# Kernel optimization log

Hardware: AMD Instinct MI355X
Metric: run time of the kernel (lower is better)

The kernel has to match this reference:

```python
import jax, jax.numpy as jnp
import numpy as np


def setup_inputs() -> dict:
    key = jax.random.key(0)
    k1, k2, k3, k4 = jax.random.split(key, 4)
    B, N, dim, heads, dim_head = 4, 1025, 768, 12, 64
    inner = heads * dim_head
    x = jax.random.normal(k1, (B, N, dim), dtype=jnp.float32)
    # binary occlusion mask over the N-1 patch tokens (CLS handled inside forward)
    mask = (jax.random.uniform(k2, (B, N - 1, dim)) > 0.5).astype(jnp.float32)
    w_qkv = jax.random.normal(k3, (inner * 3, dim), dtype=jnp.float32) * 0.02
    w_out = jax.random.normal(k4, (dim, inner), dtype=jnp.float32) * 0.02
    b_out = jnp.zeros((dim,), dtype=jnp.float32)
    return {"x": x, "mask": mask, "w_qkv": w_qkv, "w_out": w_out, "b_out": b_out, "heads": heads}


def reference(x, mask, w_qkv, w_out, b_out, heads):
    B, N, dim = x.shape
    inner = w_qkv.shape[0] // 3
    d = inner // heads
    scale = d ** -0.5

    def split_heads(t):  # [B, n, h*d] -> [B, h, n, d]
        return t.reshape(B, t.shape[1], heads, d).transpose(0, 2, 1, 3)

    qkv = x @ w_qkv.T  # [B, N, 3*inner]
    q, k, v = map(split_heads, jnp.split(qkv, 3, axis=-1))

    # --- mask propagation (torch.no_grad block) ---
    mask_sg = jax.lax.stop_gradient(mask)
    qkv_m = mask_sg @ jax.lax.stop_gradient(jnp.abs(w_qkv)).T  # [B, N-1, 3*inner]

    def norm_mask(t):
        t = split_heads(t)  # [B, h, N-1, d]
        t = t / (1e-6 + jnp.max(t, axis=2, keepdims=True))
        return jnp.concatenate([jnp.ones_like(t[:, :, :1]), t], axis=2)  # [B, h, N, d]

    q_m, k_m, v_m = map(norm_mask, jnp.split(qkv_m, 3, axis=-1))
    updated = (jnp.mean(mask_sg, axis=-1, keepdims=True) > 0.0).astype(x.dtype)  # [B, N-1, 1]
    updated = jnp.concatenate([jnp.ones_like(updated[:, :1]), updated], axis=1)  # [B, N, 1]

    # --- masked attention ---
    dots = jnp.einsum('bhnd,bhmd->bhnm', q * q_m, k * k_m) * scale
    attn = jax.nn.softmax(dots, axis=-1)
    out = jnp.einsum('bhnm,bhmd->bhnd', attn, v_m * v)
    out = out.transpose(0, 2, 1, 3).reshape(B, N, inner) * updated
    out = out @ w_out.T + b_out

    # --- mask output propagation (no grad) ---
    m = jax.lax.stop_gradient(jnp.einsum('bhnm,bhmd->bhnd', attn, v_m))
    m = m.transpose(0, 2, 1, 3).reshape(B, N, inner) * updated
    m = m @ jax.lax.stop_gradient(jnp.abs(w_out)).T
    return (out, m[:, 1:])
```

## Files before the change

### kernel.cpp

```cpp
#include <hip/hip_runtime.h>
#include <cmath>

#define TPB 256

static const int NTOK  = 1025;
static const int DIM   = 768;
static const int HEADS = 12;
static const int QK3   = 2304;
static const int ROWS  = 4 * NTOK;
static const int MROWS = 4 * (NTOK - 1);
static const int MPAD  = 4224;
static const int NPAD  = 1088;
static const size_t OUT0 = (size_t)ROWS * DIM;
static const size_t APLANE = (size_t)MPAD * DIM;

static const size_t OFF_QKV16  = 0;
static const size_t OFF_QKVM16 = 4800000;
static const size_t OFF_QE     = 9600000;
static const size_t OFF_KF     = 11300000;
static const size_t OFF_VF     = 13000000;
static const size_t OFF_ABF    = 16400000;
static const size_t OFF_WQ     = 19700000;
static const size_t OFF_WO     = 21500000;
static const size_t OFF_CMAX   = 22100000;
static const size_t OFF_UPD    = 22110000;

typedef __attribute__((ext_vector_type(8))) short short8;
typedef __attribute__((ext_vector_type(4))) float f32x4;

__device__ __forceinline__ unsigned short f2bf(float f) {
    union { float f; unsigned int u; } c; c.f = f;
    unsigned int u = c.u + 0x7fffu + ((c.u >> 16) & 1u);
    return (unsigned short)(u >> 16);
}
__device__ __forceinline__ float bf2f(unsigned short u) {
    union { unsigned int u; float f; } c; c.u = (unsigned int)u << 16;
    return c.f;
}
__device__ __forceinline__ unsigned int cvtpk(float a, float b) {
    unsigned int r;
    asm("v_cvt_pk_bf16_f32 %0, %1, %2" : "=v"(r) : "v"(a), "v"(b));
    return r;
}
__device__ __forceinline__ void gl_lds16(const unsigned short* g, unsigned short* l) {
    __builtin_amdgcn_global_load_lds(
        (const __attribute__((address_space(1))) unsigned int*)g,
        (__attribute__((address_space(3))) unsigned int*)l, 16, 0, 0);
}

__global__ __launch_bounds__(TPB)
void k_cvt(const float* __restrict__ x, const float* __restrict__ mask,
           const float* __restrict__ wqkv, const float* __restrict__ wout,
           unsigned short* __restrict__ Abf, unsigned short* __restrict__ Wq,
           unsigned short* __restrict__ Wo)
{
    const int z = blockIdx.z;
    const size_t idx = ((size_t)blockIdx.x * TPB + threadIdx.x) * 8;
    unsigned short o[8] __attribute__((aligned(16)));
    if (z <= 1) {
        if (idx >= APLANE) return;
        const int row = (int)(idx / DIM);
        const int M = z ? MROWS : ROWS;
        const float* src = z ? mask : x;
        if (row < M) {
            float a[8];
            *(float4*)&a[0] = *(const float4*)(src + idx);
            *(float4*)&a[4] = *(const float4*)(src + idx + 4);
#pragma unroll
            for (int i = 0; i < 8; ++i) o[i] = f2bf(a[i]);
        } else {
#pragma unroll
            for (int i = 0; i < 8; ++i) o[i] = 0;
        }
        *(short8*)(Abf + (size_t)z * APLANE + idx) = *(short8*)o;
    } else {
        const size_t tot = (z == 2) ? (size_t)QK3 * DIM : (size_t)DIM * DIM;
        if (idx >= tot) return;
        const float* src = (z == 2) ? wqkv : wout;
        unsigned short* dst = (z == 2) ? Wq : Wo;
        float a[8];
        *(float4*)&a[0] = *(const float4*)(src + idx);
        *(float4*)&a[4] = *(const float4*)(src + idx + 4);
        unsigned short oa[8] __attribute__((aligned(16)));
#pragma unroll
        for (int i = 0; i < 8; ++i) { o[i] = f2bf(a[i]); oa[i] = f2bf(fabsf(a[i])); }
        *(short8*)(dst + idx) = *(short8*)o;
        *(short8*)(dst + tot + idx) = *(short8*)oa;
    }
}

__global__ __launch_bounds__(TPB)
void k_gemm_qkv_mfma(const unsigned short* __restrict__ Abf,
                     const unsigned short* __restrict__ Wq,
                     unsigned short* __restrict__ qkv16,
                     unsigned short* __restrict__ qkvm16,
                     float* __restrict__ cmax)
{
    const int bid = blockIdx.x;
    const int xcd = bid & 7, rr = bid >> 3;
    const int id = (xcd < 4) ? (xcd * 149 + rr) : (596 + (xcd - 4) * 148 + rr);
    const int z = id / 594;
    const int rem = id - z * 594;
    const int by = rem / 18, bx = rem - by * 18;
    const int rowT = by * 128, colT = bx * 128;
    if (z == 1 && rowT >= MROWS) return;
    const unsigned short* A = Abf + (size_t)z * APLANE;
    const unsigned short* B = Wq + (size_t)z * QK3 * DIM;

    __shared__ unsigned short As[2][128 * 64];
    __shared__ unsigned short Bs[2][128 * 64];

    const int t = threadIdx.x;
    const int w = t >> 6, lane = t & 63, l15 = lane & 15, quad = lane >> 4;
    const int wm = (w & 1) * 64, wn = (w >> 1) * 64;
    const int sr = t >> 2, sk = (t & 3) * 8;

    f32x4 acc[4][4];
#pragma unroll
    for (int i = 0; i < 4; ++i)
#pragma unroll
        for (int j = 0; j < 4; ++j) acc[i][j] = (f32x4){0.f, 0.f, 0.f, 0.f};

    auto stage = [&](int buf, int k0) {
#pragma unroll
        for (int c = 0; c < 4; ++c) {
            const int gr = sr + (c & 1) * 64;
            const int gk = k0 + (c >> 1) * 32 + sk;
            gl_lds16(A + (size_t)(rowT + gr) * DIM + gk, As[buf] + c * 2048 + t * 8);
            gl_lds16(B + (size_t)(colT + gr) * DIM + gk, Bs[buf] + c * 2048 + t * 8);
        }
    };

    stage(0, 0);
    for (int kt = 0; kt < 12; ++kt) {
        const int cur = kt & 1;
        if (kt < 11) {
            stage(cur ^ 1, (kt + 1) * 64);
            asm volatile("s_waitcnt vmcnt(8)" ::: "memory");
        } else {
            asm volatile("s_waitcnt vmcnt(0)" ::: "memory");
        }
        __builtin_amdgcn_s_barrier();
        __builtin_amdgcn_sched_barrier(0);
        short8 fa[2][4], fb[2][4];
#pragma unroll
        for (int kk = 0; kk < 2; ++kk) {
#pragma unroll
            for (int mi = 0; mi < 4; ++mi)
                fa[kk][mi] = *(const short8*)(As[cur] + kk * 4096 + (wm + mi * 16 + l15) * 32 + quad * 8);
#pragma unroll
            for (int ni = 0; ni < 4; ++ni)
                fb[kk][ni] = *(const short8*)(Bs[cur] + kk * 4096 + (wn + ni * 16 + l15) * 32 + quad * 8);
        }
        __builtin_amdgcn_s_setprio(1);
#pragma unroll
        for (int kk = 0; kk < 2; ++kk)
#pragma unroll
            for (int mi = 0; mi < 4; ++mi)
#pragma unroll
                for (int ni = 0; ni < 4; ++ni)
                    acc[mi][ni] = __builtin_amdgcn_mfma_f32_16x16x32_bf16(fa[kk][mi], fb[kk][ni], acc[mi][ni], 0, 0, 0);
        __builtin_amdgcn_s_setprio(0);
        asm volatile("s_waitcnt lgkmcnt(0)" ::: "memory");
        __builtin_amdgcn_s_barrier();
    }

    float cm[4] = {0.f, 0.f, 0.f, 0.f};
#pragma unroll
    for (int mi = 0; mi < 4; ++mi)
#pragma unroll
        for (int ni = 0; ni < 4; ++ni) {
            const int col = colT + wn + ni * 16 + l15;
#pragma unroll
            for (int r = 0; r < 4; ++r) {
                const int row = rowT + wm + mi * 16 + quad * 4 + r;
                const float v = acc[mi][ni][r];
                if (z == 0) {
                    if (row < ROWS) qkv16[(size_t)row * QK3 + col] = f2bf(v);
                } else {
                    qkvm16[(size_t)row * QK3 + col] = f2bf(v);
                    cm[ni] = fmaxf(cm[ni], v);
                }
            }
        }
    if (z == 1) {
        const int bb = rowT >> 10;
#pragma unroll
        for (int ni = 0; ni < 4; ++ni) {
            float m = cm[ni];
            m = fmaxf(m, __shfl_xor(m, 16, 64));
            m = fmaxf(m, __shfl_xor(m, 32, 64));
            if (quad == 0)
                atomicMax((int*)&cmax[bb * QK3 + colT + wn + ni * 16 + l15], __float_as_int(m));
        }
    }
}

__global__ __launch_bounds__(TPB)
void k_misc(const float* __restrict__ mask, float* __restrict__ upd)
{
    const int bx = blockIdx.x;
    const int w = threadIdx.x >> 6, lane = threadIdx.x & 63;
    const int r = bx * 4 + w;
    if (r >= ROWS) return;
    const int b = r / NTOK, n = r % NTOK;
    float res = 1.f;
    if (n > 0) {
        const float* p = mask + (size_t)(b * (NTOK - 1) + (n - 1)) * DIM;
        float s = 0.f;
        for (int i = lane; i < DIM; i += 64) s += p[i];
#pragma unroll
        for (int off = 32; off > 0; off >>= 1) s += __shfl_xor(s, off, 64);
        res = (s > 0.f) ? 1.f : 0.f;
    }
    if (lane == 0) upd[r] = res;
}

__global__ __launch_bounds__(TPB)
void k_prep(const unsigned short* __restrict__ qkv16,
            const unsigned short* __restrict__ qkvm16,
            const float* __restrict__ cmax, unsigned short* __restrict__ qe,
            unsigned short* __restrict__ kfrag, unsigned short* __restrict__ vfrag)
{
    __shared__ unsigned short Vt_l[128 * 66];
    const int t = threadIdx.x;
    const int nt = blockIdx.x, h = blockIdx.y, b = blockIdx.z;
    const int bh = b * HEADS + h;
    const int nl = t >> 2, ds0 = (t & 3) * 16;
    const int n = nt * 64 + nl;
    const bool valid = n < NTOK;
    const int col0 = h * 64 + ds0;

    unsigned short q16[16] __attribute__((aligned(16))) = {0};
    unsigned short k16[16] __attribute__((aligned(16))) = {0};
    unsigned short v16[16] __attribute__((aligned(16))) = {0};
    unsigned short qm16[16] __attribute__((aligned(16)));
    unsigned short km16[16] __attribute__((aligned(16)));
    unsigned short vm16[16] __attribute__((aligned(16)));
    float cq[16], ck[16], cv[16];

    const bool useM = valid && (n > 0);
    if (valid) {
        const size_t br = (size_t)(b * NTOK + n) * QK3 + col0;
        *(short8*)&q16[0] = *(const short8*)(qkv16 + br);
        *(short8*)&q16[8] = *(const short8*)(qkv16 + br + 8);
        *(short8*)&k16[0] = *(const short8*)(qkv16 + br + 768);
        *(short8*)&k16[8] = *(const short8*)(qkv16 + br + 776);
        *(short8*)&v16[0] = *(const short8*)(qkv16 + br + 1536);
        *(short8*)&v16[8] = *(const short8*)(qkv16 + br + 1544);
    }
    if (useM) {
        const size_t mr = (size_t)(b * 1024 + (n - 1)) * QK3 + col0;
        *(short8*)&qm16[0] = *(const short8*)(qkvm16 + mr);
        *(short8*)&qm16[8] = *(const short8*)(qkvm16 + mr + 8);
        *(short8*)&km16[0] = *(const short8*)(qkvm16 + mr + 768);
        *(short8*)&km16[8] = *(const short8*)(qkvm16 + mr + 776);
        *(short8*)&vm16[0] = *(const short8*)(qkvm16 + mr + 1536);
        *(short8*)&vm16[8] = *(const short8*)(qkvm16 + mr + 1544);
        const int cb = b * QK3 + col0;
#pragma unroll
        for (int i = 0; i < 4; ++i) {
            *(float4*)&cq[i * 4] = *(const float4*)(cmax + cb + i * 4);
            *(float4*)&ck[i * 4] = *(const float4*)(cmax + cb + 768 + i * 4);
            *(float4*)&cv[i * 4] = *(const float4*)(cmax + cb + 1536 + i * 4);
        }
    }

    unsigned short oq[16] __attribute__((aligned(16)));
    unsigned short ok[16] __attribute__((aligned(16)));
#pragma unroll
    for (int idx = 0; idx < 16; ++idx) {
        const float qm = useM ? bf2f(qm16[idx]) / (1e-6f + cq[idx]) : 1.f;
        const float km = useM ? bf2f(km16[idx]) / (1e-6f + ck[idx]) : 1.f;
        const float vm = valid ? (useM ? bf2f(vm16[idx]) / (1e-6f + cv[idx]) : 1.f) : 0.f;
        oq[idx] = f2bf(bf2f(q16[idx]) * qm * 0.18033688f);
        ok[idx] = f2bf(bf2f(k16[idx]) * km);
        const int d = ds0 + idx;
        Vt_l[d * 66 + nl]        = f2bf(bf2f(v16[idx]) * vm);
        Vt_l[(64 + d) * 66 + nl] = f2bf(vm);
    }
    {
        unsigned short* qp = qe + ((size_t)bh * NPAD + n) * 64 + ds0;
        *(short8*)qp       = *(short8*)oq;
        *(short8*)(qp + 8) = *(short8*)(oq + 8);
    }
    {
        const int nc = nl >> 4, l15 = nl & 15;
        const int kk = ds0 >> 5, qb = (ds0 & 31) >> 3;
        unsigned short* kp = kfrag + (((size_t)bh * 17 + nt) * 8 + kk * 4 + nc) * 512;
        *(short8*)(kp + ((size_t)(qb * 16 + l15)) * 8)       = *(short8*)ok;
        *(short8*)(kp + ((size_t)((qb + 1) * 16 + l15)) * 8) = *(short8*)(ok + 8);
    }
    __syncthreads();
    const int c = t >> 1, nh = (t & 1) * 32;
    unsigned short ov[32] __attribute__((aligned(16)));
#pragma unroll
    for (int i = 0; i < 32; ++i) ov[i] = Vt_l[c * 66 + nh + i];
    const int c8 = c >> 4, l15v = c & 15, kkv = nh >> 5;
    unsigned short* vp = vfrag + (((size_t)bh * 17 + nt) * 16 + c8 * 2 + kkv) * 512 + (size_t)l15v * 8;
#pragma unroll
    for (int qd = 0; qd < 4; ++qd)
        *(short8*)(vp + (size_t)qd * 128) = *(short8*)(ov + qd * 8);
}

__global__ __launch_bounds__(64, 2)
void k_attn(const unsigned short* __restrict__ qe, const unsigned short* __restrict__ kfrag,
            const unsigned short* __restrict__ vfrag, const float* __restrict__ upd,
            unsigned short* __restrict__ ab2)
{
    const int flat = blockIdx.y * 33 + blockIdx.x;
    const int d2 = (flat & 7) * 198 + (flat >> 3);
    const int bh = d2 / 33, qt = d2 - bh * 33;
    const int b = bh / HEADS, h = bh - b * HEADS;
    const int lane = threadIdx.x;
    const int l15 = lane & 15, quad = lane >> 4;
    const int q0 = qt * 32;

    short8 qf[2][2];
#pragma unroll
    for (int j = 0; j < 2; ++j) {
        const unsigned short* qp = qe + ((size_t)bh * NPAD + q0 + j * 16 + l15) * 64 + (quad << 3);
        qf[j][0] = *(const short8*)qp;
        qf[j][1] = *(const short8*)(qp + 32);
    }
    const int pA = (quad & 1) * 32 + l15;
    const int pB = pA + 16;
    const bool lo32 = (lane < 32);

    const unsigned short* kb = kfrag + (size_t)bh * (17 * 8 * 512) + (size_t)lane * 8;
    const unsigned short* vb = vfrag + (size_t)bh * (17 * 16 * 512) + (size_t)lane * 8;

    short8 kf[8], vf[16];
#pragma unroll
    for (int g = 0; g < 8; ++g) kf[g] = *(const short8*)(kb + g * 512);
#pragma unroll
    for (int g = 0; g < 16; ++g) vf[g] = *(const short8*)(vb + g * 512);

    f32x4 acc[2][8];
    float lac[2] = {0.f, 0.f};
#pragma unroll
    for (int j = 0; j < 2; ++j)
#pragma unroll
        for (int g = 0; g < 8; ++g) acc[j][g] = (f32x4){0.f, 0.f, 0.f, 0.f};

    const float EC = 14.4269504f;

#pragma clang loop unroll(disable)
    for (int kt = 0; kt < 17; ++kt) {
        f32x4 s[2][4];
        __builtin_amdgcn_s_setprio(1);
#pragma unroll
        for (int nc = 0; nc < 4; ++nc) {
#pragma unroll
            for (int j = 0; j < 2; ++j) {
                f32x4 z = (f32x4){0.f, 0.f, 0.f, 0.f};
                z = __builtin_amdgcn_mfma_f32_16x16x32_bf16(kf[nc], qf[j][0], z, 0, 0, 0);
                z = __builtin_amdgcn_mfma_f32_16x16x32_bf16(kf[4 + nc], qf[j][1], z, 0, 0, 0);
                s[j][nc] = z;
            }
        }
        __builtin_amdgcn_s_setprio(0);
        if (kt < 16) {
            const unsigned short* kn = kb + (size_t)(kt + 1) * 4096;
#pragma unroll
            for (int g = 0; g < 8; ++g) kf[g] = *(const short8*)(kn + g * 512);
        }
        short8 pf[2][2];
#pragma unroll
        for (int j = 0; j < 2; ++j) {
            unsigned int dA[4], dB[4];
            float psum = 0.f, p00 = 0.f;
#pragma unroll
            for (int nc = 0; nc < 4; ++nc) {
                const float p0 = __builtin_amdgcn_exp2f(s[j][nc][0] - EC);
                const float p1 = __builtin_amdgcn_exp2f(s[j][nc][1] - EC);
                const float p2 = __builtin_amdgcn_exp2f(s[j][nc][2] - EC);
                const float p3 = __builtin_amdgcn_exp2f(s[j][nc][3] - EC);
                dA[nc] = cvtpk(p0, p1);
                dB[nc] = cvtpk(p2, p3);
                psum += (p0 + p1) + (p2 + p3);
                if (nc == 0) p00 = p0;
            }
            if (kt < 16) lac[j] += psum;
            else if (quad == 0) lac[j] += p00;
            union { int i[4]; short8 s; } u0, u1;
            {
                const int a0 = __shfl((int)dA[0], pA, 64), a1 = __shfl((int)dA[1], pA, 64);
                const int b0 = __shfl((int)dB[0], pA, 64), b1 = __shfl((int)dB[1], pA, 64);
                const int a2 = __shfl((int)dA[0], pB, 64), a3 = __shfl((int)dA[1], pB, 64);
                const int b2 = __shfl((int)dB[0], pB, 64), b3 = __shfl((int)dB[1], pB, 64);
                u0.i[0] = lo32 ? a0 : a1;
                u0.i[1] = lo32 ? b0 : b1;
                u0.i[2] = lo32 ? a2 : a3;
                u0.i[3] = lo32 ? b2 : b3;
            }
            {
                const int a0 = __shfl((int)dA[2], pA, 64), a1 = __shfl((int)dA[3], pA, 64);
                const int b0 = __shfl((int)dB[2], pA, 64), b1 = __shfl((int)dB[3], pA, 64);
                const int a2 = __shfl((int)dA[2], pB, 64), a3 = __shfl((int)dA[3], pB, 64);
                const int b2 = __shfl((int)dB[2], pB, 64), b3 = __shfl((int)dB[3], pB, 64);
                u1.i[0] = lo32 ? a0 : a1;
                u1.i[1] = lo32 ? b0 : b1;
                u1.i[2] = lo32 ? a2 : a3;
                u1.i[3] = lo32 ? b2 : b3;
            }
            pf[j][0] = u0.s;
            pf[j][1] = u1.s;
        }
        __builtin_amdgcn_s_setprio(1);
#pragma unroll
        for (int g = 0; g < 8; ++g) {
#pragma unroll
            for (int j = 0; j < 2; ++j) {
                acc[j][g] = __builtin_amdgcn_mfma_f32_16x16x32_bf16(vf[2 * g],     pf[j][0], acc[j][g], 0, 0, 0);
                acc[j][g] = __builtin_amdgcn_mfma_f32_16x16x32_bf16(vf[2 * g + 1], pf[j][1], acc[j][g], 0, 0, 0);
            }
        }
        __builtin_amdgcn_s_setprio(0);
        if (kt < 16) {
            const unsigned short* vn = vb + (size_t)(kt + 1) * 8192;
#pragma unroll
            for (int g = 0; g < 16; ++g) vf[g] = *(const short8*)(vn + g * 512);
        }
    }

#pragma unroll
    for (int j = 0; j < 2; ++j) {
        float lq = lac[j];
        lq += __shfl_xor(lq, 16, 64);
        lq += __shfl_xor(lq, 32, 64);
        const int qrow = q0 + j * 16 + l15;
        if (qrow < NTOK) {
            const size_t rg = (size_t)b * NTOK + qrow;
            const float inv = upd[rg] / lq;
#pragma unroll
            for (int g = 0; g < 8; ++g) {
                uint2 pk;
                pk.x = cvtpk(acc[j][g][0] * inv, acc[j][g][1] * inv);
                pk.y = cvtpk(acc[j][g][2] * inv, acc[j][g][3] * inv);
                const size_t addr = (size_t)(g >> 2) * APLANE + rg * DIM + h * 64 + (g & 3) * 16 + quad * 4;
                *(uint2*)(ab2 + addr) = pk;
            }
        }
    }
}

__global__ __launch_bounds__(TPB)
void k_gemm_out_mfma(const unsigned short* __restrict__ ab2,
                     const unsigned short* __restrict__ Wo,
                     const float* __restrict__ bout, float* __restrict__ dout)
{
    const int bid = blockIdx.x;
    const int xcd = bid & 7, rr = bid >> 3;
    const int id = (xcd < 4) ? (xcd * 50 + rr) : (200 + (xcd - 4) * 49 + rr);
    const int z = id / 198;
    const int rem = id - z * 198;
    const int by = rem / 6, bx = rem - by * 6;
    const int rowT = by * 128, colT = bx * 128;

    const unsigned short* A = ab2 + (size_t)z * APLANE;
    const unsigned short* B = Wo + (size_t)z * DIM * DIM;

    __shared__ unsigned short As[2][128 * 32];
    __shared__ unsigned short Bs[2][128 * 32];

    const int t = threadIdx.x;
    const int w = t >> 6, lane = t & 63, l15 = lane & 15, quad = lane >> 4;
    const int wm = (w & 1) * 64, wn = (w >> 1) * 64;

    const int r0 = t >> 2, kc = (t & 3) * 8;
    const unsigned short* Ap = A + (size_t)(rowT + r0) * DIM + kc;
    const unsigned short* Bp = B + (size_t)(colT + r0) * DIM + kc;

    f32x4 acc[4][4];
#pragma unroll
    for (int i = 0; i < 4; ++i)
#pragma unroll
        for (int j = 0; j < 4; ++j) acc[i][j] = (f32x4){0.f, 0.f, 0.f, 0.f};

    auto stage = [&](int buf, int k0) {
        gl_lds16(Ap + k0,            As[buf] + t * 8);
        gl_lds16(Ap + 64 * DIM + k0, As[buf] + (t + 256) * 8);
        gl_lds16(Bp + k0,            Bs[buf] + t * 8);
        gl_lds16(Bp + 64 * DIM + k0, Bs[buf] + (t + 256) * 8);
    };

    stage(0, 0);
    for (int kt = 0; kt < 24; ++kt) {
        const int cur = kt & 1;
        if (kt < 23) {
            stage(cur ^ 1, (kt + 1) * 32);
            asm volatile("s_waitcnt vmcnt(4)" ::: "memory");
        } else {
            asm volatile("s_waitcnt vmcnt(0)" ::: "memory");
        }
        __builtin_amdgcn_s_barrier();
        __builtin_amdgcn_sched_barrier(0);
        short8 fa[4], fb[4];
#pragma unroll
        for (int mi = 0; mi < 4; ++mi)
            fa[mi] = *(const short8*)(As[cur] + (wm + mi * 16 + l15) * 32 + quad * 8);
#pragma unroll
        for (int ni = 0; ni < 4; ++ni)
            fb[ni] = *(const short8*)(Bs[cur] + (wn + ni * 16 + l15) * 32 + quad * 8);
        __builtin_amdgcn_s_setprio(1);
#pragma unroll
        for (int mi = 0; mi < 4; ++mi)
#pragma unroll
            for (int ni = 0; ni < 4; ++ni)
                acc[mi][ni] = __builtin_amdgcn_mfma_f32_16x16x32_bf16(fa[mi], fb[ni], acc[mi][ni], 0, 0, 0);
        __builtin_amdgcn_s_setprio(0);
        asm volatile("s_waitcnt lgkmcnt(0)" ::: "memory");
        __builtin_amdgcn_s_barrier();
    }
#pragma unroll
    for (int mi = 0; mi < 4; ++mi)
#pragma unroll
        for (int ni = 0; ni < 4; ++ni) {
            const int col = colT + wn + ni * 16 + l15;
            const float bb = (z == 0) ? bout[col] : 0.f;
#pragma unroll
            for (int r = 0; r < 4; ++r) {
                const int row = rowT + wm + mi * 16 + quad * 4 + r;
                if (row >= ROWS) continue;
                const int b = row / NTOK, n = row % NTOK;
                if (z == 0) {
                    dout[(size_t)row * DIM + col] = acc[mi][ni][r] + bb;
                } else if (n >= 1) {
                    dout[OUT0 + ((size_t)(b * (NTOK - 1) + (n - 1))) * DIM + col] = acc[mi][ni][r];
                }
            }
        }
}

extern "C" void kernel_launch(void* const* d_in, const int* in_sizes, int n_in,
                              void* d_out, int out_size, void* d_ws, size_t ws_size,
                              hipStream_t stream)
{
    const float* x    = (const float*)d_in[0];
    const float* mask = (const float*)d_in[1];
    const float* wqkv = (const float*)d_in[2];
    const float* wout = (const float*)d_in[3];
    const float* bout = (const float*)d_in[4];
    float* ws = (float*)d_ws;
    unsigned short* qkv16  = (unsigned short*)(ws + OFF_QKV16);
    unsigned short* qkvm16 = (unsigned short*)(ws + OFF_QKVM16);
    unsigned short* qe  = (unsigned short*)(ws + OFF_QE);
    unsigned short* kfr = (unsigned short*)(ws + OFF_KF);
    unsigned short* vfr = (unsigned short*)(ws + OFF_VF);
    unsigned short* abf = (unsigned short*)(ws + OFF_ABF);
    unsigned short* wq  = (unsigned short*)(ws + OFF_WQ);
    unsigned short* wo  = (unsigned short*)(ws + OFF_WO);
    float* cmax = ws + OFF_CMAX;
    float* upd  = ws + OFF_UPD;
    float* out  = (float*)d_out;

    hipMemsetAsync(cmax, 0, 9216 * sizeof(float), stream);
    hipLaunchKernelGGL(k_cvt,           dim3(1584, 1, 4), dim3(TPB), 0, stream, x, mask, wqkv, wout, abf, wq, wo);
    hipLaunchKernelGGL(k_gemm_qkv_mfma, dim3(1188),       dim3(TPB), 0, stream, abf, wq, qkv16, qkvm16, cmax);
    hipLaunchKernelGGL(k_misc,          dim3(1025),       dim3(TPB), 0, stream, mask, upd);
    hipLaunchKernelGGL(k_prep,          dim3(17, 12, 4),  dim3(TPB), 0, stream, qkv16, qkvm16, cmax, qe, kfr, vfr);
    hipLaunchKernelGGL(k_attn,          dim3(33, 48),     dim3(64),  0, stream, qe, kfr, vfr, upd, abf);
    hipLaunchKernelGGL(k_gemm_out_mfma, dim3(396),        dim3(TPB), 0, stream, abf, wo, bout, out);
}
```

Baseline: 223.3 us.

## Load GEMM fragments directly from global into registers, dropping LDS staging

Both the QKV and output-projection GEMM kernels drop their LDS double-buffered staging (global_load_lds plus barriers). Each wave now loads its MFMA A/B fragments straight from global memory into registers, using a two-register-set software pipeline over K in steps of 64. This removes the LDS traffic and block-wide barriers. In exchange, every wave fetches its own operand rows, so there is no sharing across the block and more global/L2 traffic, and register pressure rises from holding two fragment sets.

```diff
diff --git a/kernel.cpp b/kernel.cpp
--- a/kernel.cpp
+++ b/kernel.cpp
@@ -41,11 +41,6 @@
     unsigned int r;
     asm("v_cvt_pk_bf16_f32 %0, %1, %2" : "=v"(r) : "v"(a), "v"(b));
     return r;
-}
-__device__ __forceinline__ void gl_lds16(const unsigned short* g, unsigned short* l) {
-    __builtin_amdgcn_global_load_lds(
-        (const __attribute__((address_space(1))) unsigned int*)g,
-        (__attribute__((address_space(3))) unsigned int*)l, 16, 0, 0);
 }
 
 __global__ __launch_bounds__(TPB)
@@ -107,13 +102,12 @@
     const unsigned short* A = Abf + (size_t)z * APLANE;
     const unsigned short* B = Wq + (size_t)z * QK3 * DIM;
 
-    __shared__ unsigned short As[2][128 * 64];
-    __shared__ unsigned short Bs[2][128 * 64];
-
     const int t = threadIdx.x;
     const int w = t >> 6, lane = t & 63, l15 = lane & 15, quad = lane >> 4;
     const int wm = (w & 1) * 64, wn = (w >> 1) * 64;
-    const int sr = t >> 2, sk = (t & 3) * 8;
+
+    const unsigned short* pa = A + (size_t)(rowT + wm + l15) * DIM + quad * 8;
+    const unsigned short* pb = B + (size_t)(colT + wn + l15) * DIM + quad * 8;
 
     f32x4 acc[4][4];
 #pragma unroll
@@ -121,48 +115,37 @@
 #pragma unroll
         for (int j = 0; j < 4; ++j) acc[i][j] = (f32x4){0.f, 0.f, 0.f, 0.f};
 
-    auto stage = [&](int buf, int k0) {
-#pragma unroll
-        for (int c = 0; c < 4; ++c) {
-            const int gr = sr + (c & 1) * 64;
-            const int gk = k0 + (c >> 1) * 32 + sk;
-            gl_lds16(A + (size_t)(rowT + gr) * DIM + gk, As[buf] + c * 2048 + t * 8);
-            gl_lds16(B + (size_t)(colT + gr) * DIM + gk, Bs[buf] + c * 2048 + t * 8);
-        }
+    short8 fa0[8], fb0[8], fa1[8], fb1[8];
+
+    auto lset = [&](short8* fa, short8* fb, int k0) {
+#pragma unroll
+        for (int kk = 0; kk < 2; ++kk)
+#pragma unroll
+            for (int mi = 0; mi < 4; ++mi) {
+                fa[kk * 4 + mi] = *(const short8*)(pa + (size_t)mi * 16 * DIM + k0 + kk * 32);
+                fb[kk * 4 + mi] = *(const short8*)(pb + (size_t)mi * 16 * DIM + k0 + kk * 32);
+            }
     };
-
-    stage(0, 0);
-    for (int kt = 0; kt < 12; ++kt) {
-        const int cur = kt & 1;
-        if (kt < 11) {
-            stage(cur ^ 1, (kt + 1) * 64);
-            asm volatile("s_waitcnt vmcnt(8)" ::: "memory");
-        } else {
-            asm volatile("s_waitcnt vmcnt(0)" ::: "memory");
-        }
-        __builtin_amdgcn_s_barrier();
-        __builtin_amdgcn_sched_barrier(0);
-        short8 fa[2][4], fb[2][4];
-#pragma unroll
-        for (int kk = 0; kk < 2; ++kk) {
+    auto mm = [&](const short8* fa, const short8* fb) {
+        __builtin_amdgcn_s_setprio(1);
+#pragma unroll
+        for (int kk = 0; kk < 2; ++kk)
 #pragma unroll
             for (int mi = 0; mi < 4; ++mi)
-                fa[kk][mi] = *(const short8*)(As[cur] + kk * 4096 + (wm + mi * 16 + l15) * 32 + quad * 8);
-#pragma unroll
-            for (int ni = 0; ni < 4; ++ni)
-                fb[kk][ni] = *(const short8*)(Bs[cur] + kk * 4096 + (wn + ni * 16 + l15) * 32 + quad * 8);
-        }
-        __builtin_amdgcn_s_setprio(1);
-#pragma unroll
-        for (int kk = 0; kk < 2; ++kk)
-#pragma unroll
-            for (int mi = 0; mi < 4; ++mi)
 #pragma unroll
                 for (int ni = 0; ni < 4; ++ni)
-                    acc[mi][ni] = __builtin_amdgcn_mfma_f32_16x16x32_bf16(fa[kk][mi], fb[kk][ni], acc[mi][ni], 0, 0, 0);
+                    acc[mi][ni] = __builtin_amdgcn_mfma_f32_16x16x32_bf16(
+                        fa[kk * 4 + mi], fb[kk * 4 + ni], acc[mi][ni], 0, 0, 0);
         __builtin_amdgcn_s_setprio(0);
-        asm volatile("s_waitcnt lgkmcnt(0)" ::: "memory");
-        __builtin_amdgcn_s_barrier();
+    };
+
+    lset(fa0, fb0, 0);
+#pragma clang loop unroll(disable)
+    for (int kt = 0; kt < 12; kt += 2) {
+        if (kt + 1 < 12) lset(fa1, fb1, (kt + 1) * 64);
+        mm(fa0, fb0);
+        if (kt + 2 < 12) lset(fa0, fb0, (kt + 2) * 64);
+        mm(fa1, fb1);
     }
 
     float cm[4] = {0.f, 0.f, 0.f, 0.f};
@@ -461,16 +444,12 @@
     const unsigned short* A = ab2 + (size_t)z * APLANE;
     const unsigned short* B = Wo + (size_t)z * DIM * DIM;
 
-    __shared__ unsigned short As[2][128 * 32];
-    __shared__ unsigned short Bs[2][128 * 32];
-
     const int t = threadIdx.x;
     const int w = t >> 6, lane = t & 63, l15 = lane & 15, quad = lane >> 4;
     const int wm = (w & 1) * 64, wn = (w >> 1) * 64;
 
-    const int r0 = t >> 2, kc = (t & 3) * 8;
-    const unsigned short* Ap = A + (size_t)(rowT + r0) * DIM + kc;
-    const unsigned short* Bp = B + (size_t)(colT + r0) * DIM + kc;
+    const unsigned short* pa = A + (size_t)(rowT + wm + l15) * DIM + quad * 8;
+    const unsigned short* pb = B + (size_t)(colT + wn + l15) * DIM + quad * 8;
 
     f32x4 acc[4][4];
 #pragma unroll
@@ -478,41 +457,39 @@
 #pragma unroll
         for (int j = 0; j < 4; ++j) acc[i][j] = (f32x4){0.f, 0.f, 0.f, 0.f};
 
-    auto stage = [&](int buf, int k0) {
-        gl_lds16(Ap + k0,            As[buf] + t * 8);
-        gl_lds16(Ap + 64 * DIM + k0, As[buf] + (t + 256) * 8);
-        gl_lds16(Bp + k0,            Bs[buf] + t * 8);
-        gl_lds16(Bp + 64 * DIM + k0, Bs[buf] + (t + 256) * 8);
+    short8 fa0[8], fb0[8], fa1[8], fb1[8];
+
+    auto lset = [&](short8* fa, short8* fb, int k0) {
+#pragma unroll
+        for (int kk = 0; kk < 2; ++kk)
+#pragma unroll
+            for (int mi = 0; mi < 4; ++mi) {
+                fa[kk * 4 + mi] = *(const short8*)(pa + (size_t)mi * 16 * DIM + k0 + kk * 32);
+                fb[kk * 4 + mi] = *(const short8*)(pb + (size_t)mi * 16 * DIM + k0 + kk * 32);
+            }
     };
-
-    stage(0, 0);
-    for (int kt = 0; kt < 24; ++kt) {
-        const int cur = kt & 1;
-        if (kt < 23) {
-            stage(cur ^ 1, (kt + 1) * 32);
-            asm volatile("s_waitcnt vmcnt(4)" ::: "memory");
-        } else {
-            asm volatile("s_waitcnt vmcnt(0)" ::: "memory");
-        }
-        __builtin_amdgcn_s_barrier();
-        __builtin_amdgcn_sched_barrier(0);
-        short8 fa[4], fb[4];
-#pragma unroll
-        for (int mi = 0; mi < 4; ++mi)
-            fa[mi] = *(const short8*)(As[cur] + (wm + mi * 16 + l15) * 32 + quad * 8);
-#pragma unroll
-        for (int ni = 0; ni < 4; ++ni)
-            fb[ni] = *(const short8*)(Bs[cur] + (wn + ni * 16 + l15) * 32 + quad * 8);
+    auto mm = [&](const short8* fa, const short8* fb) {
         __builtin_amdgcn_s_setprio(1);
 #pragma unroll
-        for (int mi = 0; mi < 4; ++mi)
-#pragma unroll
-            for (int ni = 0; ni < 4; ++ni)
-                acc[mi][ni] = __builtin_amdgcn_mfma_f32_16x16x32_bf16(fa[mi], fb[ni], acc[mi][ni], 0, 0, 0);
+        for (int kk = 0; kk < 2; ++kk)
+#pragma unroll
+            for (int mi = 0; mi < 4; ++mi)
+#pragma unroll
+                for (int ni = 0; ni < 4; ++ni)
+                    acc[mi][ni] = __builtin_amdgcn_mfma_f32_16x16x32_bf16(
+                        fa[kk * 4 + mi], fb[kk * 4 + ni], acc[mi][ni], 0, 0, 0);
         __builtin_amdgcn_s_setprio(0);
-        asm volatile("s_waitcnt lgkmcnt(0)" ::: "memory");
-        __builtin_amdgcn_s_barrier();
-    }
+    };
+
+    lset(fa0, fb0, 0);
+#pragma clang loop unroll(disable)
+    for (int kt = 0; kt < 12; kt += 2) {
+        if (kt + 1 < 12) lset(fa1, fb1, (kt + 1) * 64);
+        mm(fa0, fb0);
+        if (kt + 2 < 12) lset(fa0, fb0, (kt + 2) * 64);
+        mm(fa1, fb1);
+    }
+
 #pragma unroll
     for (int mi = 0; mi < 4; ++mi)
 #pragma unroll
```

New measurement: 316.3 us. +41.7%, slower.
